# Kernel tuning notes

Measured on AMD Instinct MI355X. Metric: run time of the kernel, lower is better.

The kernel has to match this reference:

```python
import jax, jax.numpy as jnp
import numpy as np

B, S1, S2, E, P = 8, 2048, 2048, 1024, 1024


def setup_inputs() -> dict:
    key = jax.random.key(0)
    k1, k2, k3, k4, k5 = jax.random.split(key, 5)
    query = jax.random.normal(k1, (B, S1, E), dtype=jnp.float32)
    key_t = jax.random.normal(k2, (B, S2, E), dtype=jnp.float32)
    value = jax.random.normal(k3, (B, S2, E), dtype=jnp.float32)
    # nn.Linear(E, P): weight (P, E), bias (P), shared by q/k/v per the source
    bound = 1.0 / np.sqrt(E)
    W = jax.random.uniform(k4, (P, E), minval=-bound, maxval=bound, dtype=jnp.float32)
    b = jax.random.uniform(k5, (P,), minval=-bound, maxval=bound, dtype=jnp.float32)
    return {"query": query, "key": key_t, "value": value, "W": W, "b": b}


def reference(query, key, value, W, b):
    # Source applies queries_projection to all three inputs.
    q = jnp.einsum("bse,pe->bsp", query, W) + b  # (B,S1,P)
    k = jnp.einsum("bse,pe->bsp", key, W) + b    # (B,S2,P)
    v = jnp.einsum("bse,pe->bsp", value, W) + b  # (B,S2,P)
    scale = 1.0 / jnp.sqrt(jnp.float32(k.shape[-1]))
    scores = jnp.einsum("bqp,bkp->bqk", q, k) * scale  # (B,S1,S2)
    weights = jax.nn.softmax(scores, axis=-1)
    return jnp.einsum("bqk,bkp->bqp", weights, v)  # (B,S1,P)
```

## Files before the change

kernel.cpp:

```cpp
#include <hip/hip_runtime.h>


typedef unsigned short u16;
typedef __bf16 bf16x8 __attribute__((ext_vector_type(8)));
typedef float f32x4 __attribute__((ext_vector_type(4)));

__device__ __forceinline__ float b2f(u16 u) {
    union { unsigned i; float f; } x; x.i = ((unsigned)u) << 16; return x.f;
}
__device__ __forceinline__ u16 f2b(float f) {
    union { float f; unsigned i; } x; x.f = f;
    unsigned r = x.i + 0x7FFFu + ((x.i >> 16) & 1u);
    return (u16)(r >> 16);
}

__global__ __launch_bounds__(256)
void convert_all(const float* __restrict__ q, const float* __restrict__ k,
                 const float* __restrict__ v, const float* __restrict__ W,
                 const float* __restrict__ bias,
                 u16* __restrict__ xq, u16* __restrict__ xk,
                 u16* __restrict__ xv, u16* __restrict__ Wc,
                 u16* __restrict__ bc)
{
    const long b = blockIdx.x;
    const float* src; u16* dst; long off; long n;
    if (b < 8192)       { src = q;    dst = xq; off = b;         n = 16777216L; }
    else if (b < 16384) { src = k;    dst = xk; off = b - 8192;  n = 16777216L; }
    else if (b < 24576) { src = v;    dst = xv; off = b - 16384; n = 16777216L; }
    else if (b < 25088) { src = W;    dst = Wc; off = b - 24576; n = 1048576L;  }
    else                { src = bias; dst = bc; off = 0;         n = 1024L;     }
    const long i = (off * 256 + threadIdx.x) * 8;
    if (i >= n) return;
    const float4* s = (const float4*)(src + i);
    float4 a = s[0], c = s[1];
    ushort4 lo, hi;
    lo.x = f2b(a.x); lo.y = f2b(a.y); lo.z = f2b(a.z); lo.w = f2b(a.w);
    hi.x = f2b(c.x); hi.y = f2b(c.y); hi.z = f2b(c.z); hi.w = f2b(c.w);
    *(ushort4*)(dst + i) = lo;
    *(ushort4*)(dst + i + 4) = hi;
}


#define BARX()   __builtin_amdgcn_s_barrier()
#define WAITL0() asm volatile("s_waitcnt lgkmcnt(0)" ::: "memory")
#define WV4()    asm volatile("s_waitcnt vmcnt(4)" ::: "memory")
#define WV0()    asm volatile("s_waitcnt vmcnt(0)" ::: "memory")
#define PRIO1()  __builtin_amdgcn_s_setprio(1)
#define PRIO0()  __builtin_amdgcn_s_setprio(0)

__global__ __launch_bounds__(512, 2)
void gemm8(const u16* __restrict__ A0, const u16* __restrict__ A1,
           const u16* __restrict__ A2, const u16* __restrict__ B,
           void* __restrict__ C, const u16* __restrict__ bias,
           int K, float alpha, int em, int ldc,
           long zA, long zB, long zC, int rmap, int pw, int ph)
{
    __shared__ __align__(16) u16 lds[65536];

    int tx = blockIdx.x, ty = blockIdx.y, z = blockIdx.z;
    if (rmap == 2) {
        const int g = tx + ty * 4 + z * 256;
        const int xcd = g & 7, i = g >> 3;
        const int G = xcd * 24 + (i >> 2);
        tx = i & 3; z = G >> 6; ty = G & 63;
    } else if (rmap == 3) {
        const int gx = gridDim.x;
        const int lin = ty * gx + tx;
        const int xcd = lin & 7, i = lin >> 3;
        const int pcols = gx / pw;
        const int pr = xcd / pcols, pc = xcd - pr * pcols;
        tx = pc * pw + (i % pw);
        ty = pr * ph + (i / pw);
    }

    const int eff5 = (em == 5);
    const u16* Ap = eff5 ? (z == 0 ? A0 : (z == 1 ? A1 : A2)) : A0 + zA * z;
    const u16* Bp = B + zB * z;
    const long coff = zC * z;
    const int eme = eff5 ? (z == 2 ? 2 : 0) : em;

    const int bm0 = ty << 8, bn0 = tx << 8;

    const int tid = threadIdx.x;
    const int wave = tid >> 6, lane = tid & 63;
    const int wm = wave >> 2, wn = wave & 3;
    const int quad = lane >> 4, l15 = lane & 15;
    const int sw = l15 & 7;

    const int srow = (wave << 3) + (lane >> 3);
    const int sgc  = (((lane & 7) ^ (lane >> 3)) << 3);
    const int sdst = (wave << 9) + (lane << 3);

#define STG_A(b, h, kt) do {                                                          \
    _Pragma("unroll")                                                                 \
    for (int q_ = 0; q_ < 2; ++q_)                                                    \
        __builtin_amdgcn_global_load_lds(                                             \
            (const __attribute__((address_space(1))) void*)(                          \
                Ap + (long)(bm0 + (h)*128 + q_*64 + srow) * K + (kt) + sgc),          \
            (__attribute__((address_space(3))) void*)(                                \
                lds + (b)*32768 + ((h)*128 + q_*64)*64 + sdst),                       \
            16, 0, 0);                                                                \
} while (0)

#define STG_B(b, h, kt) do {                                                          \
    _Pragma("unroll")                                                                 \
    for (int q_ = 0; q_ < 2; ++q_)                                                    \
        __builtin_amdgcn_global_load_lds(                                             \
            (const __attribute__((address_space(1))) void*)(                          \
                Bp + (long)(bn0 + (h)*128 + q_*64 + srow) * K + (kt) + sgc),          \
            (__attribute__((address_space(3))) void*)(                                \
                lds + (b)*32768 + 16384 + ((h)*128 + q_*64)*64 + sdst),               \
            16, 0, 0);                                                                \
} while (0)

#define LDA(b, m, kk) (*(const bf16x8*)(lds + (b)*32768 +                             \
    ((wm << 7) + ((m) << 4) + l15) * 64 + (((((kk) << 2) + quad) ^ sw) << 3)))
#define LDB(b, n, kk) (*(const bf16x8*)(lds + (b)*32768 + 16384 +                     \
    ((wn << 6) + ((n) << 4) + l15) * 64 + (((((kk) << 2) + quad) ^ sw) << 3)))

#define RD_A(b, mh) do {                                                              \
    _Pragma("unroll") for (int mr = 0; mr < 4; ++mr)                                  \
    _Pragma("unroll") for (int kk = 0; kk < 2; ++kk)                                  \
        af[mr][kk] = LDA(b, (mh)*4 + mr, kk);                                         \
} while (0)
#define RD_B(b, nh) do {                                                              \
    _Pragma("unroll") for (int j = 0; j < 2; ++j)                                     \
    _Pragma("unroll") for (int kk = 0; kk < 2; ++kk)                                  \
        bq[nh][j][kk] = LDB(b, (nh)*2 + j, kk);                                       \
} while (0)

#define MMAQ(mh, nh) do {                                                             \
    _Pragma("unroll") for (int mr = 0; mr < 4; ++mr)                                  \
    _Pragma("unroll") for (int j = 0; j < 2; ++j)                                     \
    _Pragma("unroll") for (int kk = 0; kk < 2; ++kk)                                  \
        acc[(mh)*4 + mr][(nh)*2 + j] = __builtin_amdgcn_mfma_f32_16x16x32_bf16(       \
            af[mr][kk], bq[nh][j][kk], acc[(mh)*4 + mr][(nh)*2 + j], 0, 0, 0);        \
} while (0)

    f32x4 acc[8][4];
#pragma unroll
    for (int m = 0; m < 8; ++m)
#pragma unroll
        for (int n = 0; n < 4; ++n) acc[m][n] = f32x4{0.f, 0.f, 0.f, 0.f};

    bf16x8 af[4][2];
    bf16x8 bq[2][2][2];

    STG_B(0, 0, 0); STG_B(0, 1, 0);
    STG_A(0, 0, 0); STG_A(0, 1, 0);
    STG_B(1, 0, 64); STG_B(1, 1, 64);
    WV4(); BARX();

    const int NI = K >> 7;
    for (int i = 0; i < NI - 1; ++i) {
        const int kt0 = i << 7;
        const int kt1 = kt0 + 64, kt2 = kt0 + 128, kt3 = kt0 + 192;
        RD_A(0, 0); RD_B(0, 0); STG_A(1, 0, kt1);
        BARX(); WAITL0(); PRIO1(); MMAQ(0, 0); PRIO0(); BARX();
        RD_B(0, 1); STG_A(1, 1, kt1);
        BARX(); WAITL0(); PRIO1(); MMAQ(0, 1); PRIO0(); BARX();
        RD_A(0, 1); STG_B(0, 0, kt2);
        BARX(); WAITL0(); PRIO1(); MMAQ(1, 0); PRIO0(); BARX();
        STG_B(0, 1, kt2);
        BARX(); PRIO1(); MMAQ(1, 1); PRIO0(); WV4(); BARX();
        RD_A(1, 0); RD_B(1, 0); STG_A(0, 0, kt2);
        BARX(); WAITL0(); PRIO1(); MMAQ(0, 0); PRIO0(); BARX();
        RD_B(1, 1); STG_A(0, 1, kt2);
        BARX(); WAITL0(); PRIO1(); MMAQ(0, 1); PRIO0(); BARX();
        RD_A(1, 1); STG_B(1, 0, kt3);
        BARX(); WAITL0(); PRIO1(); MMAQ(1, 0); PRIO0(); BARX();
        STG_B(1, 1, kt3);
        BARX(); PRIO1(); MMAQ(1, 1); PRIO0(); WV4(); BARX();
    }
    {
        const int kt1 = ((NI - 1) << 7) + 64;
        RD_A(0, 0); RD_B(0, 0); STG_A(1, 0, kt1);
        BARX(); WAITL0(); PRIO1(); MMAQ(0, 0); PRIO0(); BARX();
        RD_B(0, 1); STG_A(1, 1, kt1);
        BARX(); WAITL0(); PRIO1(); MMAQ(0, 1); PRIO0(); BARX();
        RD_A(0, 1);
        BARX(); WAITL0(); PRIO1(); MMAQ(1, 0); PRIO0(); BARX();
        PRIO1(); MMAQ(1, 1); PRIO0(); WV0(); BARX();
        RD_A(1, 0); RD_B(1, 0);
        BARX(); WAITL0(); PRIO1(); MMAQ(0, 0); PRIO0(); BARX();
        RD_B(1, 1);
        BARX(); WAITL0(); PRIO1(); MMAQ(0, 1); PRIO0(); BARX();
        RD_A(1, 1);
        BARX(); WAITL0(); PRIO1(); MMAQ(1, 0); PRIO0(); BARX();
        PRIO1(); MMAQ(1, 1); PRIO0();
    }

#pragma unroll
    for (int m = 0; m < 8; ++m) {
        const int row = bm0 + (wm << 7) + (m << 4) + (quad << 2);
#pragma unroll
        for (int n = 0; n < 4; ++n) {
            const int col = bn0 + (wn << 6) + (n << 4) + l15;
            const float bv = bias ? b2f(bias[col]) : 0.f;
            f32x4 v = acc[m][n];
            const float o0 = alpha * v[0] + bv;
            const float o1 = alpha * v[1] + bv;
            const float o2 = alpha * v[2] + bv;
            const float o3 = alpha * v[3] + bv;
            if (eme == 2) {
                ushort4 pk;
                pk.x = f2b(o0); pk.y = f2b(o1); pk.z = f2b(o2); pk.w = f2b(o3);
                *(ushort4*)((u16*)C + coff + ((long)(row >> 11) << 21)
                            + ((long)col << 11) + (row & 2047)) = pk;
            } else if (eme == 1) {
                float* Cf = (float*)C + coff;
                Cf[(long)(row + 0) * ldc + col] = o0;
                Cf[(long)(row + 1) * ldc + col] = o1;
                Cf[(long)(row + 2) * ldc + col] = o2;
                Cf[(long)(row + 3) * ldc + col] = o3;
            } else {
                u16* Cb = (u16*)C + coff;
                Cb[(long)(row + 0) * ldc + col] = f2b(o0);
                Cb[(long)(row + 1) * ldc + col] = f2b(o1);
                Cb[(long)(row + 2) * ldc + col] = f2b(o2);
                Cb[(long)(row + 3) * ldc + col] = f2b(o3);
            }
        }
    }
}

__global__ __launch_bounds__(256)
void softmax_rows(u16* __restrict__ S)
{
    const long row = blockIdx.x;
    u16* p = S + (row << 11);
    const int tid = threadIdx.x, wave = tid >> 6, lane = tid & 63;

    union { uint4 q; u16 u[8]; } d;
    d.q = ((const uint4*)p)[tid];
    float v[8];
#pragma unroll
    for (int i = 0; i < 8; i++) v[i] = b2f(d.u[i]);

    float m = v[0];
#pragma unroll
    for (int i = 1; i < 8; i++) m = fmaxf(m, v[i]);
#pragma unroll
    for (int o = 32; o; o >>= 1) m = fmaxf(m, __shfl_xor(m, o, 64));
    __shared__ float redm[4], reds[4];
    if (lane == 0) redm[wave] = m;
    __syncthreads();
    m = fmaxf(fmaxf(redm[0], redm[1]), fmaxf(redm[2], redm[3]));

    float e[8], s = 0.f;
#pragma unroll
    for (int i = 0; i < 8; i++) { e[i] = __expf(v[i] - m); s += e[i]; }
#pragma unroll
    for (int o = 32; o; o >>= 1) s += __shfl_xor(s, o, 64);
    if (lane == 0) reds[wave] = s;
    __syncthreads();
    s = reds[0] + reds[1] + reds[2] + reds[3];

    const float inv = 1.f / s;
#pragma unroll
    for (int i = 0; i < 8; i++) d.u[i] = f2b(e[i] * inv);
    ((uint4*)p)[tid] = d.q;
}

extern "C" void kernel_launch(void* const* d_in, const int* in_sizes, int n_in,
                              void* d_out, int out_size, void* d_ws, size_t ws_size,
                              hipStream_t stream) {
    const float* query = (const float*)d_in[0];
    const float* key   = (const float*)d_in[1];
    const float* value = (const float*)d_in[2];
    const float* W     = (const float*)d_in[3];
    const float* bias  = (const float*)d_in[4];
    float* out = (float*)d_out;

    u16* sc  = (u16*)d_ws;
    u16* xq  = (u16*)d_ws;
    u16* xk  = (u16*)d_ws + 16777216L;
    u16* qb  = (u16*)d_ws + 33554432L;
    u16* kb  = qb + 16777216L;
    u16* vT  = kb + 16777216L;
    u16* xv  = (u16*)d_out;
    u16* Wc  = (u16*)d_out + 16777216L;
    u16* bc  = Wc + 1048576L;

    const dim3 blk2(256), blk5(512);

    convert_all<<<dim3(25089), blk2, 0, stream>>>(query, key, value, W, bias,
                                                  xq, xk, xv, Wc, bc);

    gemm8<<<dim3(4, 64, 3), blk5, 0, stream>>>(xq, xk, xv, Wc, qb, bc,
        1024, 1.f, 5, 1024, 0, 0, 16777216L, 2, 0, 0);

    gemm8<<<dim3(8, 8, 8), blk5, 0, stream>>>(qb, nullptr, nullptr, kb, sc, nullptr,
        1024, 0.03125f, 0, 2048, 2048L * 1024, 2048L * 1024, 2048L * 2048, 3, 8, 1);

    softmax_rows<<<dim3(16384), blk2, 0, stream>>>(sc);

    gemm8<<<dim3(4, 8, 8), blk5, 0, stream>>>(sc, nullptr, nullptr, vT, out, nullptr,
        2048, 1.f, 1, 1024, 2048L * 2048, 1024L * 2048, 2048L * 1024, 3, 4, 1);
}
```

Measured before the change: 503.1 us.

## Triple-buffer A tiles in LDS to deepen the GEMM prefetch pipeline

LDS grows from 128KB to 160KB so the A operand gets three rotating 32KB buffers while B stays double-buffered. The prologue now prefetches two A tiles, the loop rotates the A buffer offsets, and the vmcnt wait rises from 4 to 8 so more global-to-LDS loads stay in flight. The aim is to hide global load latency behind MFMA work, at the cost of more LDS per block, which may cut occupancy below the 2 blocks per CU set in launch_bounds.

```diff
diff --git a/kernel.cpp b/kernel.cpp
--- a/kernel.cpp
+++ b/kernel.cpp
@@ -43,7 +43,7 @@
 
 #define BARX()   __builtin_amdgcn_s_barrier()
 #define WAITL0() asm volatile("s_waitcnt lgkmcnt(0)" ::: "memory")
-#define WV4()    asm volatile("s_waitcnt vmcnt(4)" ::: "memory")
+#define WV8()    asm volatile("s_waitcnt vmcnt(8)" ::: "memory")
 #define WV0()    asm volatile("s_waitcnt vmcnt(0)" ::: "memory")
 #define PRIO1()  __builtin_amdgcn_s_setprio(1)
 #define PRIO0()  __builtin_amdgcn_s_setprio(0)
@@ -55,7 +55,7 @@
            int K, float alpha, int em, int ldc,
            long zA, long zB, long zC, int rmap, int pw, int ph)
 {
-    __shared__ __align__(16) u16 lds[65536];
+    __shared__ __align__(16) u16 lds[81920];
 
     int tx = blockIdx.x, ty = blockIdx.y, z = blockIdx.z;
     if (rmap == 2) {
@@ -91,42 +91,42 @@
     const int sgc  = (((lane & 7) ^ (lane >> 3)) << 3);
     const int sdst = (wave << 9) + (lane << 3);
 
-#define STG_A(b, h, kt) do {                                                          \
+#define STG_A(ab, h, kt) do {                                                         \
     _Pragma("unroll")                                                                 \
     for (int q_ = 0; q_ < 2; ++q_)                                                    \
         __builtin_amdgcn_global_load_lds(                                             \
             (const __attribute__((address_space(1))) void*)(                          \
                 Ap + (long)(bm0 + (h)*128 + q_*64 + srow) * K + (kt) + sgc),          \
             (__attribute__((address_space(3))) void*)(                                \
-                lds + (b)*32768 + ((h)*128 + q_*64)*64 + sdst),                       \
+                lds + (ab) + ((h)*128 + q_*64)*64 + sdst),                            \
             16, 0, 0);                                                                \
 } while (0)
 
-#define STG_B(b, h, kt) do {                                                          \
+#define STG_B(bb, h, kt) do {                                                         \
     _Pragma("unroll")                                                                 \
     for (int q_ = 0; q_ < 2; ++q_)                                                    \
         __builtin_amdgcn_global_load_lds(                                             \
             (const __attribute__((address_space(1))) void*)(                          \
                 Bp + (long)(bn0 + (h)*128 + q_*64 + srow) * K + (kt) + sgc),          \
             (__attribute__((address_space(3))) void*)(                                \
-                lds + (b)*32768 + 16384 + ((h)*128 + q_*64)*64 + sdst),               \
+                lds + 49152 + (bb)*16384 + ((h)*128 + q_*64)*64 + sdst),              \
             16, 0, 0);                                                                \
 } while (0)
 
-#define LDA(b, m, kk) (*(const bf16x8*)(lds + (b)*32768 +                             \
+#define LDA(ab, m, kk) (*(const bf16x8*)(lds + (ab) +                                 \
     ((wm << 7) + ((m) << 4) + l15) * 64 + (((((kk) << 2) + quad) ^ sw) << 3)))
-#define LDB(b, n, kk) (*(const bf16x8*)(lds + (b)*32768 + 16384 +                     \
+#define LDB(bb, n, kk) (*(const bf16x8*)(lds + 49152 + (bb)*16384 +                   \
     ((wn << 6) + ((n) << 4) + l15) * 64 + (((((kk) << 2) + quad) ^ sw) << 3)))
 
-#define RD_A(b, mh) do {                                                              \
+#define RD_A(ab, mh) do {                                                             \
     _Pragma("unroll") for (int mr = 0; mr < 4; ++mr)                                  \
     _Pragma("unroll") for (int kk = 0; kk < 2; ++kk)                                  \
-        af[mr][kk] = LDA(b, (mh)*4 + mr, kk);                                         \
-} while (0)
-#define RD_B(b, nh) do {                                                              \
+        af[mr][kk] = LDA(ab, (mh)*4 + mr, kk);                                        \
+} while (0)
+#define RD_B(bb, nh) do {                                                             \
     _Pragma("unroll") for (int j = 0; j < 2; ++j)                                     \
     _Pragma("unroll") for (int kk = 0; kk < 2; ++kk)                                  \
-        bq[nh][j][kk] = LDB(b, (nh)*2 + j, kk);                                       \
+        bq[nh][j][kk] = LDB(bb, (nh)*2 + j, kk);                                      \
 } while (0)
 
 #define MMAQ(mh, nh) do {                                                             \
@@ -146,46 +146,47 @@
     bf16x8 af[4][2];
     bf16x8 bq[2][2][2];
 
-    STG_B(0, 0, 0); STG_B(0, 1, 0);
-    STG_A(0, 0, 0); STG_A(0, 1, 0);
-    STG_B(1, 0, 64); STG_B(1, 1, 64);
-    WV4(); BARX();
-
+    STG_A(0, 0, 0);      STG_A(0, 1, 0);
+    STG_B(0, 0, 0);      STG_B(0, 1, 0);
+    STG_A(16384, 0, 64); STG_A(16384, 1, 64);
+    STG_B(1, 0, 64);     STG_B(1, 1, 64);
+    WV8(); BARX();
+
+    int a0 = 0, a1 = 16384, a2 = 32768;
     const int NI = K >> 7;
     for (int i = 0; i < NI - 1; ++i) {
-        const int kt0 = i << 7;
-        const int kt1 = kt0 + 64, kt2 = kt0 + 128, kt3 = kt0 + 192;
-        RD_A(0, 0); RD_B(0, 0); STG_A(1, 0, kt1);
+        const int kt2 = (i << 7) + 128, kt3 = kt2 + 64;
+        RD_A(a0, 0); RD_B(0, 0); STG_A(a2, 0, kt2);
         BARX(); WAITL0(); PRIO1(); MMAQ(0, 0); PRIO0(); BARX();
-        RD_B(0, 1); STG_A(1, 1, kt1);
+        RD_B(0, 1); STG_A(a2, 1, kt2);
         BARX(); WAITL0(); PRIO1(); MMAQ(0, 1); PRIO0(); BARX();
-        RD_A(0, 1); STG_B(0, 0, kt2);
+        RD_A(a0, 1); STG_B(0, 0, kt2);
         BARX(); WAITL0(); PRIO1(); MMAQ(1, 0); PRIO0(); BARX();
         STG_B(0, 1, kt2);
-        BARX(); PRIO1(); MMAQ(1, 1); PRIO0(); WV4(); BARX();
-        RD_A(1, 0); RD_B(1, 0); STG_A(0, 0, kt2);
+        BARX(); PRIO1(); MMAQ(1, 1); PRIO0(); WV8(); BARX();
+        RD_A(a1, 0); RD_B(1, 0); STG_A(a0, 0, kt3);
         BARX(); WAITL0(); PRIO1(); MMAQ(0, 0); PRIO0(); BARX();
-        RD_B(1, 1); STG_A(0, 1, kt2);
+        RD_B(1, 1); STG_A(a0, 1, kt3);
         BARX(); WAITL0(); PRIO1(); MMAQ(0, 1); PRIO0(); BARX();
-        RD_A(1, 1); STG_B(1, 0, kt3);
+        RD_A(a1, 1); STG_B(1, 0, kt3);
         BARX(); WAITL0(); PRIO1(); MMAQ(1, 0); PRIO0(); BARX();
         STG_B(1, 1, kt3);
-        BARX(); PRIO1(); MMAQ(1, 1); PRIO0(); WV4(); BARX();
+        BARX(); PRIO1(); MMAQ(1, 1); PRIO0(); WV8(); BARX();
+        const int tmp = a2; a2 = a1; a1 = a0; a0 = tmp;
     }
     {
-        const int kt1 = ((NI - 1) << 7) + 64;
-        RD_A(0, 0); RD_B(0, 0); STG_A(1, 0, kt1);
+        RD_A(a0, 0); RD_B(0, 0);
         BARX(); WAITL0(); PRIO1(); MMAQ(0, 0); PRIO0(); BARX();
-        RD_B(0, 1); STG_A(1, 1, kt1);
+        RD_B(0, 1);
         BARX(); WAITL0(); PRIO1(); MMAQ(0, 1); PRIO0(); BARX();
-        RD_A(0, 1);
+        RD_A(a0, 1);
         BARX(); WAITL0(); PRIO1(); MMAQ(1, 0); PRIO0(); BARX();
         PRIO1(); MMAQ(1, 1); PRIO0(); WV0(); BARX();
-        RD_A(1, 0); RD_B(1, 0);
+        RD_A(a1, 0); RD_B(1, 0);
         BARX(); WAITL0(); PRIO1(); MMAQ(0, 0); PRIO0(); BARX();
         RD_B(1, 1);
         BARX(); WAITL0(); PRIO1(); MMAQ(0, 1); PRIO0(); BARX();
-        RD_A(1, 1);
+        RD_A(a1, 1);
         BARX(); WAITL0(); PRIO1(); MMAQ(1, 0); PRIO0(); BARX();
         PRIO1(); MMAQ(1, 1); PRIO0();
     }
```

After: 487.9 us. 1.03x faster.
